# Kernel tuning notes

Hardware: AMD Instinct MI355X
Metric: run time of the kernel (lower is better)

Reference implementation:

```python
import jax, jax.numpy as jnp
import numpy as np

T, B, C, H, K = 2048, 4, 1024, 16, 7  # timesteps, batch, channels, heads, kernel
R = C // H  # channels per head


def setup_inputs() -> dict:
    key = jax.random.key(0)
    k1, k2 = jax.random.split(key)
    x = jax.random.normal(k1, (T, B, C), dtype=jnp.float32)
    # xavier_uniform for weight_linear: shape (H*K, C), fan_in=C, fan_out=H*K
    a = float(np.sqrt(6.0 / (C + H * K)))
    W = jax.random.uniform(k2, (H * K, C), dtype=jnp.float32, minval=-a, maxval=a)
    conv_bias = jnp.zeros((C,), dtype=jnp.float32)
    return {"x": x, "W": W, "conv_bias": conv_bias}


def reference(x, W, conv_bias):
    Tn, Bn, Cn = x.shape
    Kn, Hn = K, H
    Rn = Cn // Hn
    # dynamic filters predicted from the input itself (query = x)
    w = jnp.einsum('tbc,oc->tbo', x, W).reshape(Tn, Bn, Hn, Kn)
    w = jax.nn.softmax(w, axis=-1)  # softmax over the small kernel dim
    # causal unfold: padding_l = K-1 zeros on the left of the time axis
    x_pad = jnp.pad(x, ((Kn - 1, 0), (0, 0), (0, 0)))
    # x_unf[t, b, c, k] = x[t - (K-1) + k]  (zeros outside)
    x_unf = jnp.stack([x_pad[k:k + Tn] for k in range(Kn)], axis=-1)  # T,B,C,K
    x_unf = x_unf.reshape(Tn, Bn, Hn, Rn, Kn)
    out = jnp.einsum('tbhrk,tbhk->tbhr', x_unf, w).reshape(Tn, Bn, Cn)
    return out + conv_bias[None, None, :]
```

## Files before the change

### kernel.cpp

```cpp
#include <hip/hip_runtime.h>
#include <hip/hip_bf16.h>

#define T_DIM 2048
#define B_DIM 4
#define C_DIM 1024
#define H_DIM 16
#define K_DIM 7
#define HK    112
#define TT    16

typedef float f32x4 __attribute__((ext_vector_type(4)));
typedef short s16x8 __attribute__((ext_vector_type(8)));

__device__ __forceinline__ short f2bf(float f) {
    union { float f; unsigned u; } v; v.f = f;
    return (short)((v.u + 0x7FFFu + ((v.u >> 16) & 1u)) >> 16);
}
__device__ __forceinline__ float bf2f(unsigned short s) {
    union { unsigned u; float f; } v; v.u = ((unsigned)s) << 16; return v.f;
}

__global__ void k_cvtW(const float* __restrict__ W, short* __restrict__ Wb) {
    const int i = ((int)blockIdx.x * 256 + (int)threadIdx.x) * 8;
    f32x4 a = *(const f32x4*)(W + i);
    f32x4 b = *(const f32x4*)(W + i + 4);
    s16x8 o;
    o[0] = f2bf(a[0]); o[1] = f2bf(a[1]); o[2] = f2bf(a[2]); o[3] = f2bf(a[3]);
    o[4] = f2bf(b[0]); o[5] = f2bf(b[1]); o[6] = f2bf(b[2]); o[7] = f2bf(b[3]);
    *(s16x8*)(Wb + i) = o;
}

__global__ __launch_bounds__(256, 2) void k_logits(const float* __restrict__ x,
                                                   const short* __restrict__ Wb,
                                                   unsigned short* __restrict__ wt) {
    __shared__ float sm[4][16][113];

    const int tid  = (int)threadIdx.x;
    const int lane = tid & 63;
    const int wid  = tid >> 6;
    const int m0   = (int)blockIdx.x * 16;

    const int cl   = lane & 15;
    const int koff = (lane >> 4) * 8;

    const float* aptr = x  + (size_t)(m0 + cl) * C_DIM + koff;
    const short* bptr = Wb + (size_t)cl * C_DIM + koff;

    f32x4 acc[K_DIM];
    #pragma unroll
    for (int n = 0; n < K_DIM; ++n) acc[n] = (f32x4){0.f, 0.f, 0.f, 0.f};

    for (int q = 0; q < 8; ++q) {
        const int kb = wid * 8 + q;
        f32x4 a0 = *(const f32x4*)(aptr + kb * 32);
        f32x4 a1 = *(const f32x4*)(aptr + kb * 32 + 4);
        s16x8 afr;
        afr[0] = f2bf(a0[0]); afr[1] = f2bf(a0[1]); afr[2] = f2bf(a0[2]); afr[3] = f2bf(a0[3]);
        afr[4] = f2bf(a1[0]); afr[5] = f2bf(a1[1]); afr[6] = f2bf(a1[2]); afr[7] = f2bf(a1[3]);
        #pragma unroll
        for (int nt = 0; nt < K_DIM; ++nt) {
            s16x8 bf = *(const s16x8*)(bptr + nt * 16 * C_DIM + kb * 32);
            acc[nt] = __builtin_amdgcn_mfma_f32_16x16x32_bf16(afr, bf, acc[nt], 0, 0, 0);
        }
    }

    const int r0 = (lane >> 4) * 4;
    #pragma unroll
    for (int nt = 0; nt < K_DIM; ++nt)
        #pragma unroll
        for (int j = 0; j < 4; ++j)
            sm[wid][r0 + j][nt * 16 + cl] = acc[nt][j];
    __syncthreads();

    const int r = tid >> 4, h = tid & 15;
    float v[K_DIM];
    float mx = -1e30f;
    #pragma unroll
    for (int k = 0; k < K_DIM; ++k) {
        v[k] = sm[0][r][h * 7 + k] + sm[1][r][h * 7 + k]
             + sm[2][r][h * 7 + k] + sm[3][r][h * 7 + k];
        mx = fmaxf(mx, v[k]);
    }
    float s = 0.f;
    #pragma unroll
    for (int k = 0; k < K_DIM; ++k) { v[k] = __expf(v[k] - mx); s += v[k]; }
    const float inv = 1.f / s;
    unsigned short* wrow = wt + (size_t)(m0 + r) * HK + h * 7;
    #pragma unroll
    for (int k = 0; k < K_DIM; ++k) wrow[k] = (unsigned short)f2bf(v[k] * inv);
}

__global__ __launch_bounds__(256) void k_conv(const float* __restrict__ x,
                                              const unsigned short* __restrict__ wt,
                                              const float* __restrict__ bias,
                                              float* __restrict__ out) {
    __shared__ float smw[TT][HK];
    const int tid = (int)threadIdx.x;
    const int b   = (int)blockIdx.y;
    const int t0  = (int)blockIdx.x * TT;

    if (tid < TT * 14) {
        const int row = tid / 14, seg = tid % 14;
        const unsigned short* p = wt + ((size_t)(t0 + row) * B_DIM + b) * HK + seg * 8;
        s16x8 wv = *(const s16x8*)p;
        #pragma unroll
        for (int j = 0; j < 8; ++j)
            smw[row][seg * 8 + j] = bf2f(((const unsigned short*)&wv)[j]);
    }

    const int c4 = tid * 4;
    const int h  = tid >> 4;
    const f32x4 bias4 = *(const f32x4*)(bias + c4);

    f32x4 win[6];
    #pragma unroll
    for (int k = 0; k < 6; ++k) {
        const int t = t0 - 6 + k;
        win[k] = (t >= 0) ? *(const f32x4*)(x + ((size_t)t * B_DIM + b) * C_DIM + c4)
                          : (f32x4){0.f, 0.f, 0.f, 0.f};
    }
    __syncthreads();

    #pragma unroll
    for (int tt = 0; tt < TT; ++tt) {
        const size_t row = (size_t)(t0 + tt) * B_DIM + b;
        const f32x4 xv = *(const f32x4*)(x + row * C_DIM + c4);
        const float* wr = &smw[tt][h * 7];

        f32x4 o = bias4;
        o += win[0] * wr[0];
        o += win[1] * wr[1];
        o += win[2] * wr[2];
        o += win[3] * wr[3];
        o += win[4] * wr[4];
        o += win[5] * wr[5];
        o += xv     * wr[6];
        *(f32x4*)(out + row * C_DIM + c4) = o;

        win[0] = win[1]; win[1] = win[2]; win[2] = win[3];
        win[3] = win[4]; win[4] = win[5]; win[5] = xv;
    }
}

extern "C" void kernel_launch(void* const* d_in, const int* in_sizes, int n_in,
                              void* d_out, int out_size, void* d_ws, size_t ws_size,
                              hipStream_t stream) {
    const float* x    = (const float*)d_in[0];
    const float* W    = (const float*)d_in[1];
    const float* bias = (const float*)d_in[2];
    float* out = (float*)d_out;

    short*          Wb = (short*)d_ws;
    unsigned short* wt = (unsigned short*)((char*)d_ws + 262144);

    k_cvtW  <<<56, 256, 0, stream>>>(W, Wb);
    k_logits<<<(T_DIM * B_DIM) / 16, 256, 0, stream>>>(x, Wb, wt);
    k_conv  <<<dim3(T_DIM / TT, B_DIM), 256, 0, stream>>>(x, wt, bias, out);
}
```

Before: 107.5 us.

## Fuse logits softmax and causal conv into a single kernel

Merges the logits/softmax kernel with the convolution kernel, so the softmax weights stay in shared memory as fp32 instead of being written to a bf16 workspace and read back. Each block now covers 4 timesteps across all batches and, per batch, reloads a 10-row window of x (6 halo rows plus 4 output rows). This removes one launch and the workspace round-trip. In exchange, the halo reload fraction rises sharply because each block produces only 4 timesteps, and the launch_bounds occupancy hint is dropped.

Result: slower. 111.5 us (+3.7%).

```diff
diff --git a/kernel.cpp b/kernel.cpp
--- a/kernel.cpp
+++ b/kernel.cpp
@@ -7,7 +7,6 @@
 #define H_DIM 16
 #define K_DIM 7
 #define HK    112
-#define TT    16
 
 typedef float f32x4 __attribute__((ext_vector_type(4)));
 typedef short s16x8 __attribute__((ext_vector_type(8)));
@@ -15,9 +14,6 @@
 __device__ __forceinline__ short f2bf(float f) {
     union { float f; unsigned u; } v; v.f = f;
     return (short)((v.u + 0x7FFFu + ((v.u >> 16) & 1u)) >> 16);
-}
-__device__ __forceinline__ float bf2f(unsigned short s) {
-    union { unsigned u; float f; } v; v.u = ((unsigned)s) << 16; return v.f;
 }
 
 __global__ void k_cvtW(const float* __restrict__ W, short* __restrict__ Wb) {
@@ -30,15 +26,18 @@
     *(s16x8*)(Wb + i) = o;
 }
 
-__global__ __launch_bounds__(256, 2) void k_logits(const float* __restrict__ x,
-                                                   const short* __restrict__ Wb,
-                                                   unsigned short* __restrict__ wt) {
+__global__ __launch_bounds__(256) void k_fused(const float* __restrict__ x,
+                                               const short* __restrict__ Wb,
+                                               const float* __restrict__ bias,
+                                               float* __restrict__ out) {
     __shared__ float sm[4][16][113];
+    __shared__ float smw[16][HK];
 
     const int tid  = (int)threadIdx.x;
     const int lane = tid & 63;
     const int wid  = tid >> 6;
     const int m0   = (int)blockIdx.x * 16;
+    const int t0   = (int)blockIdx.x * 4;
 
     const int cl   = lane & 15;
     const int koff = (lane >> 4) * 8;
@@ -72,73 +71,53 @@
             sm[wid][r0 + j][nt * 16 + cl] = acc[nt][j];
     __syncthreads();
 
-    const int r = tid >> 4, h = tid & 15;
-    float v[K_DIM];
-    float mx = -1e30f;
-    #pragma unroll
-    for (int k = 0; k < K_DIM; ++k) {
-        v[k] = sm[0][r][h * 7 + k] + sm[1][r][h * 7 + k]
-             + sm[2][r][h * 7 + k] + sm[3][r][h * 7 + k];
-        mx = fmaxf(mx, v[k]);
+    {
+        const int r = tid >> 4, h = tid & 15;
+        float v[K_DIM];
+        float mx = -1e30f;
+        #pragma unroll
+        for (int k = 0; k < K_DIM; ++k) {
+            v[k] = sm[0][r][h * 7 + k] + sm[1][r][h * 7 + k]
+                 + sm[2][r][h * 7 + k] + sm[3][r][h * 7 + k];
+            mx = fmaxf(mx, v[k]);
+        }
+        float s = 0.f;
+        #pragma unroll
+        for (int k = 0; k < K_DIM; ++k) { v[k] = __expf(v[k] - mx); s += v[k]; }
+        const float inv = 1.f / s;
+        #pragma unroll
+        for (int k = 0; k < K_DIM; ++k) smw[r][h * 7 + k] = v[k] * inv;
     }
-    float s = 0.f;
-    #pragma unroll
-    for (int k = 0; k < K_DIM; ++k) { v[k] = __expf(v[k] - mx); s += v[k]; }
-    const float inv = 1.f / s;
-    unsigned short* wrow = wt + (size_t)(m0 + r) * HK + h * 7;
-    #pragma unroll
-    for (int k = 0; k < K_DIM; ++k) wrow[k] = (unsigned short)f2bf(v[k] * inv);
-}
-
-__global__ __launch_bounds__(256) void k_conv(const float* __restrict__ x,
-                                              const unsigned short* __restrict__ wt,
-                                              const float* __restrict__ bias,
-                                              float* __restrict__ out) {
-    __shared__ float smw[TT][HK];
-    const int tid = (int)threadIdx.x;
-    const int b   = (int)blockIdx.y;
-    const int t0  = (int)blockIdx.x * TT;
-
-    if (tid < TT * 14) {
-        const int row = tid / 14, seg = tid % 14;
-        const unsigned short* p = wt + ((size_t)(t0 + row) * B_DIM + b) * HK + seg * 8;
-        s16x8 wv = *(const s16x8*)p;
-        #pragma unroll
-        for (int j = 0; j < 8; ++j)
-            smw[row][seg * 8 + j] = bf2f(((const unsigned short*)&wv)[j]);
-    }
+    __syncthreads();
 
     const int c4 = tid * 4;
     const int h  = tid >> 4;
     const f32x4 bias4 = *(const f32x4*)(bias + c4);
-
-    f32x4 win[6];
-    #pragma unroll
-    for (int k = 0; k < 6; ++k) {
-        const int t = t0 - 6 + k;
-        win[k] = (t >= 0) ? *(const f32x4*)(x + ((size_t)t * B_DIM + b) * C_DIM + c4)
-                          : (f32x4){0.f, 0.f, 0.f, 0.f};
-    }
-    __syncthreads();
+    const f32x4 zero4 = {0.f, 0.f, 0.f, 0.f};
 
     #pragma unroll
-    for (int tt = 0; tt < TT; ++tt) {
-        const size_t row = (size_t)(t0 + tt) * B_DIM + b;
-        const f32x4 xv = *(const f32x4*)(x + row * C_DIM + c4);
-        const float* wr = &smw[tt][h * 7];
-
-        f32x4 o = bias4;
-        o += win[0] * wr[0];
-        o += win[1] * wr[1];
-        o += win[2] * wr[2];
-        o += win[3] * wr[3];
-        o += win[4] * wr[4];
-        o += win[5] * wr[5];
-        o += xv     * wr[6];
-        *(f32x4*)(out + row * C_DIM + c4) = o;
-
-        win[0] = win[1]; win[1] = win[2]; win[2] = win[3];
-        win[3] = win[4]; win[4] = win[5]; win[5] = xv;
+    for (int b = 0; b < B_DIM; ++b) {
+        f32x4 rv[10];
+        #pragma unroll
+        for (int j = 0; j < 10; ++j) {
+            const int t = t0 - 6 + j;
+            rv[j] = (t >= 0)
+                  ? *(const f32x4*)(x + (size_t)(t * B_DIM + b) * C_DIM + c4)
+                  : zero4;
+        }
+        #pragma unroll
+        for (int tt = 0; tt < 4; ++tt) {
+            const float* wr = &smw[tt * 4 + b][h * 7];
+            f32x4 o = bias4;
+            o += rv[tt + 0] * wr[0];
+            o += rv[tt + 1] * wr[1];
+            o += rv[tt + 2] * wr[2];
+            o += rv[tt + 3] * wr[3];
+            o += rv[tt + 4] * wr[4];
+            o += rv[tt + 5] * wr[5];
+            o += rv[tt + 6] * wr[6];
+            *(f32x4*)(out + (size_t)((t0 + tt) * B_DIM + b) * C_DIM + c4) = o;
+        }
     }
 }
 
@@ -149,11 +128,8 @@
     const float* W    = (const float*)d_in[1];
     const float* bias = (const float*)d_in[2];
     float* out = (float*)d_out;
+    short* Wb  = (short*)d_ws;
 
-    short*          Wb = (short*)d_ws;
-    unsigned short* wt = (unsigned short*)((char*)d_ws + 262144);
-
-    k_cvtW  <<<56, 256, 0, stream>>>(W, Wb);
-    k_logits<<<(T_DIM * B_DIM) / 16, 256, 0, stream>>>(x, Wb, wt);
-    k_conv  <<<dim3(T_DIM / TT, B_DIM), 256, 0, stream>>>(x, wt, bias, out);
+    k_cvtW <<<56, 256, 0, stream>>>(W, Wb);
+    k_fused<<<(T_DIM * B_DIM) / 16, 256, 0, stream>>>(x, Wb, bias, out);
 }
```
